# Kernel tuning notes

Hardware: AMD Instinct MI355X
Metric: run time of the kernel (lower is better)

Reference implementation:

```python
import jax, jax.numpy as jnp
import numpy as np

DEPTH = 6
IN_FEATURES = 256
NUM_TREES = 256
TREE_DIM = 1
BATCH = 2048


def sparsemax(X, axis=0):
    """Full-sort sparsemax projection along `axis` (k=None path of the torch code)."""
    X = jnp.moveaxis(X, axis, -1)
    Xs = X - jnp.max(X, axis=-1, keepdims=True)
    z = -jnp.sort(-Xs, axis=-1)                      # descending sort
    cs = jnp.cumsum(z, axis=-1) - 1.0                # topk_cumsum - 1
    d = X.shape[-1]
    rho = jnp.arange(1, d + 1, dtype=X.dtype)
    support = rho * z > cs
    k = jnp.sum(support, axis=-1, keepdims=True)     # support size (int)
    tau = jnp.take_along_axis(cs, k - 1, axis=-1) / k.astype(X.dtype)
    out = jnp.maximum(Xs - tau, 0.0)
    return jnp.moveaxis(out, -1, axis)


def sparsemoid(x):
    return jnp.clip(0.5 * x + 0.5, 0.0, 1.0)


def bin_codes_1hot(depth, dtype=jnp.float32):
    idx = jnp.arange(2 ** depth)
    off = 2 ** jnp.arange(depth)
    codes = ((idx[None, :] // off[:, None]) % 2).astype(dtype)   # [depth, 2^depth]
    return jnp.stack([codes, 1.0 - codes], axis=-1)              # [depth, 2^depth, 2]


def setup_inputs() -> dict:
    key = jax.random.key(0)
    k1, k2, k3, k4, k5 = jax.random.split(key, 5)
    x = jax.random.normal(k1, (BATCH, IN_FEATURES), dtype=jnp.float32)
    response = jax.random.normal(k2, (NUM_TREES, TREE_DIM, 2 ** DEPTH), dtype=jnp.float32)
    feature_selection_logits = jax.random.uniform(k3, (IN_FEATURES, NUM_TREES, DEPTH), dtype=jnp.float32)
    feature_thresholds = 0.5 * jax.random.normal(k4, (NUM_TREES, DEPTH), dtype=jnp.float32)
    log_temperatures = jnp.zeros((NUM_TREES, DEPTH), dtype=jnp.float32)
    return {
        "x": x,
        "response": response,
        "feature_selection_logits": feature_selection_logits,
        "feature_thresholds": feature_thresholds,
        "log_temperatures": log_temperatures,
    }


def reference(x, response, feature_selection_logits, feature_thresholds, log_temperatures):
    depth = feature_thresholds.shape[-1]
    codes = bin_codes_1hot(depth, x.dtype)                          # [d, 2^d, 2]
    # sparsemax feature routing over the feature axis
    fs = sparsemax(feature_selection_logits, axis=0)                # [F, T, d]
    fv = jnp.einsum('bi,ind->bnd', x, fs)                           # [B, T, d]
    tl = (fv - feature_thresholds) * jnp.exp(-log_temperatures)     # [B, T, d]
    bins = sparsemoid(jnp.stack([-tl, tl], axis=-1))                # [B, T, d, 2]
    bin_matches = jnp.einsum('btds,dcs->btdc', bins, codes)         # [B, T, d, 2^d]
    response_weights = jnp.prod(bin_matches, axis=-2)               # [B, T, 2^d]
    out = jnp.einsum('bnd,ncd->bnc', response_weights, response)    # [B, T, C]
    return out.reshape(out.shape[0], -1)                            # flatten_output=True
```

## Files before the change

### kernel.cpp

```cpp
#include <hip/hip_runtime.h>
#include <math.h>
#include <stdint.h>

#define NF 256
#define NT 256
#define ND 6
#define NB 2048
#define NCOL (NT * ND)
#define NLEAF 64

typedef __attribute__((ext_vector_type(8))) short bf16x8;
typedef __attribute__((ext_vector_type(4))) float f32x4;
typedef __attribute__((ext_vector_type(4))) unsigned short u16x4;

__device__ inline unsigned short f2bf(float f) {
    unsigned u = __float_as_uint(f);
    u += 0x7fffu + ((u >> 16) & 1u);
    return (unsigned short)(u >> 16);
}
__device__ inline float bf2f(unsigned short h) {
    return __uint_as_float(((unsigned)h) << 16);
}

__device__ inline void gld16(const void* g, void* l) {
    __builtin_amdgcn_global_load_lds(
        (const __attribute__((address_space(1))) unsigned int*)(uintptr_t)g,
        (__attribute__((address_space(3))) unsigned int*)(uintptr_t)l,
        16, 0, 0);
}

__global__ __launch_bounds__(256) void setup_kernel(
    const float* __restrict__ fsl,
    const float* __restrict__ x,
    const float* __restrict__ lt,
    unsigned short* __restrict__ fs_hi,
    unsigned short* __restrict__ fs_lo,
    unsigned short* __restrict__ x_hi,
    unsigned short* __restrict__ x_lo,
    float* __restrict__ scl)
{
    const int tid  = threadIdx.x;
    const int lane = tid & 63;
    const int col  = blockIdx.x * 4 + (tid >> 6);

    float xv[4];
    #pragma unroll
    for (int j = 0; j < 4; j++)
        xv[j] = fsl[(lane + 64 * j) * NCOL + col];

    float mx = fmaxf(fmaxf(xv[0], xv[1]), fmaxf(xv[2], xv[3]));
    #pragma unroll
    for (int off = 32; off > 0; off >>= 1)
        mx = fmaxf(mx, __shfl_xor(mx, off));
    #pragma unroll
    for (int j = 0; j < 4; j++) xv[j] -= mx;

    float s = (xv[0] + xv[1]) + (xv[2] + xv[3]);
    #pragma unroll
    for (int off = 32; off > 0; off >>= 1)
        s += __shfl_xor(s, off);
    float tau = (s - 1.0f) / 256.0f;

    int prev = 256;
    for (int it = 0; it < 64; it++) {
        float ss = 0.0f, cc = 0.0f;
        #pragma unroll
        for (int j = 0; j < 4; j++)
            if (xv[j] > tau) { ss += xv[j]; cc += 1.0f; }
        #pragma unroll
        for (int off = 32; off > 0; off >>= 1) {
            ss += __shfl_xor(ss, off);
            cc += __shfl_xor(cc, off);
        }
        const int c = (int)cc;
        if (c == prev) break;
        prev = c;
        tau = (ss - 1.0f) / cc;
    }

    #pragma unroll
    for (int j = 0; j < 4; j++) {
        const float v = fmaxf(xv[j] - tau, 0.0f);
        const unsigned short h = f2bf(v);
        fs_hi[col * NF + lane + 64 * j] = h;
        fs_lo[col * NF + lane + 64 * j] = f2bf(v - bf2f(h));
    }

    const int gid = blockIdx.x * 256 + tid;
    for (int e = gid; e < NB * NF / 4; e += (NCOL / 4) * 256) {
        const float4 v = ((const float4*)x)[e];
        const float vv[4] = {v.x, v.y, v.z, v.w};
        u16x4 h, l;
        #pragma unroll
        for (int j = 0; j < 4; j++) {
            h[j] = f2bf(vv[j]);
            l[j] = f2bf(vv[j] - bf2f(h[j]));
        }
        ((u16x4*)x_hi)[e] = h;
        ((u16x4*)x_lo)[e] = l;
    }

    if (gid < NT * ND) scl[gid] = __expf(-lt[gid]);
}

#define TM 64
#define TN 96
#define TK 32

struct MainBuf {
    unsigned short Ah[TM * TK];
    unsigned short Al[TM * TK];
    unsigned short Bh[TN * TK];
    unsigned short Bl[TN * TK];
};

union SMem {
    MainBuf mb[2];
    struct {
        float fv[TM][TN + 1];
        float resp[16][NLEAF + 4];
        float th[16 * ND];
        float sc[16 * ND];
    } ep;
};

__global__ __launch_bounds__(256) void gemm_tree_kernel(
    const unsigned short* __restrict__ x_hi,
    const unsigned short* __restrict__ x_lo,
    const unsigned short* __restrict__ fs_hi,
    const unsigned short* __restrict__ fs_lo,
    const float* __restrict__ thr,
    const float* __restrict__ scl,
    const float* __restrict__ resp_g,
    float* __restrict__ out)
{
    __shared__ SMem sm;

    const int tid  = threadIdx.x;
    const int lane = tid & 63;
    const int w    = tid >> 6;
    const int wm   = w & 1;
    const int wn   = w >> 1;
    const int bm0  = blockIdx.y * TM;
    const int bn0  = blockIdx.x * TN;
    const int t0   = blockIdx.x * 16;

    const int l15  = lane & 15;
    const int quad = lane >> 4;

    const int lr = lane >> 2;
    const int cp = lane & 3;

    const int rA  = (w << 4) + lr;
    const int cA  = cp ^ ((rA >> 1) & 3);
    const unsigned short* pAh = x_hi + (bm0 + rA) * NF + cA * 8;
    const unsigned short* pAl = x_lo + (bm0 + rA) * NF + cA * 8;

    const int s0  = w;
    const int rB0 = (s0 << 4) + lr;
    const int cB0 = cp ^ ((rB0 >> 1) & 3);
    const unsigned short* pBh0 = fs_hi + (bn0 + rB0) * NF + cB0 * 8;
    const unsigned short* pBl0 = fs_lo + (bn0 + rB0) * NF + cB0 * 8;
    const int s1  = w + 4;
    const int rB1 = (s1 << 4) + lr;
    const int cB1 = cp ^ ((rB1 >> 1) & 3);
    const unsigned short* pBh1 = fs_hi + (bn0 + rB1) * NF + cB1 * 8;
    const unsigned short* pBl1 = fs_lo + (bn0 + rB1) * NF + cB1 * 8;

    auto stage = [&](int kb, int k0) {
        MainBuf& b = sm.mb[kb];
        gld16(pAh + k0, &b.Ah[w << 9]);
        gld16(pAl + k0, &b.Al[w << 9]);
        gld16(pBh0 + k0, &b.Bh[s0 << 9]);
        gld16(pBl0 + k0, &b.Bl[s0 << 9]);
        if (w < 2) {
            gld16(pBh1 + k0, &b.Bh[s1 << 9]);
            gld16(pBl1 + k0, &b.Bl[s1 << 9]);
        }
    };

    f32x4 acc[2][3] = {};

    stage(0, 0);
    __syncthreads();

    #pragma unroll
    for (int t = 0; t < NF / TK; ++t) {
        const int kb = t & 1;
        if (t < NF / TK - 1) stage(kb ^ 1, (t + 1) * TK);

        MainBuf& b = sm.mb[kb];
        #pragma unroll
        for (int im = 0; im < 2; im++) {
            const int ar = wm * 32 + im * 16 + l15;
            const int sa = (quad ^ ((ar >> 1) & 3)) * 8;
            const bf16x8 a_h = *(const bf16x8*)&b.Ah[ar * TK + sa];
            const bf16x8 a_l = *(const bf16x8*)&b.Al[ar * TK + sa];
            #pragma unroll
            for (int in = 0; in < 3; in++) {
                const int br = wn * 48 + in * 16 + l15;
                const int sb = (quad ^ ((br >> 1) & 3)) * 8;
                const bf16x8 b_h = *(const bf16x8*)&b.Bh[br * TK + sb];
                const bf16x8 b_l = *(const bf16x8*)&b.Bl[br * TK + sb];
                acc[im][in] = __builtin_amdgcn_mfma_f32_16x16x32_bf16(a_h, b_h, acc[im][in], 0, 0, 0);
                acc[im][in] = __builtin_amdgcn_mfma_f32_16x16x32_bf16(a_h, b_l, acc[im][in], 0, 0, 0);
                acc[im][in] = __builtin_amdgcn_mfma_f32_16x16x32_bf16(a_l, b_h, acc[im][in], 0, 0, 0);
            }
        }
        __syncthreads();
    }

    #pragma unroll
    for (int im = 0; im < 2; im++)
        #pragma unroll
        for (int in = 0; in < 3; in++)
            #pragma unroll
            for (int r = 0; r < 4; r++) {
                const int m = wm * 32 + im * 16 + quad * 4 + r;
                const int n = wn * 48 + in * 16 + l15;
                sm.ep.fv[m][n] = acc[im][in][r];
            }
    {
        const int tr  = tid >> 4;
        const int seg = (tid & 15) * 4;
        *(f32x4*)&sm.ep.resp[tr][seg] = *(const f32x4*)&resp_g[(t0 + tr) * NLEAF + seg];
    }
    if (tid < 16 * ND)       sm.ep.th[tid]      = thr[t0 * ND + tid];
    else if (tid < 32 * ND)  sm.ep.sc[tid - 96] = scl[t0 * ND + tid - 96];
    __syncthreads();

    const int t16 = tid & 15;
    const int mr  = tid >> 4;
    #pragma unroll
    for (int i = 0; i < 4; i++) {
        const int m = mr + 16 * i;

        float sp[ND], sn[ND];
        #pragma unroll
        for (int d = 0; d < ND; d++) {
            const float f  = sm.ep.fv[m][t16 * ND + d];
            const float tl = (f - sm.ep.th[t16 * ND + d]) * sm.ep.sc[t16 * ND + d];
            const float h  = 0.5f * tl;
            sp[d] = fminf(fmaxf(0.5f + h, 0.0f), 1.0f);
            sn[d] = fminf(fmaxf(0.5f - h, 0.0f), 1.0f);
        }

        float r[32];
        #pragma unroll
        for (int c = 0; c < 32; c++)
            r[c] = sp[5] * sm.ep.resp[t16][c] + sn[5] * sm.ep.resp[t16][c + 32];
        #pragma unroll
        for (int d = 4; d >= 0; d--) {
            const int half = 1 << d;
            #pragma unroll
            for (int c = 0; c < 32; c++)
                if (c < half) r[c] = sp[d] * r[c] + sn[d] * r[c + half];
        }

        out[(bm0 + m) * NT + t0 + t16] = r[0];
    }
}

extern "C" void kernel_launch(void* const* d_in, const int* in_sizes, int n_in,
                              void* d_out, int out_size, void* d_ws, size_t ws_size,
                              hipStream_t stream)
{
    const float* x    = (const float*)d_in[0];
    const float* resp = (const float*)d_in[1];
    const float* fsl  = (const float*)d_in[2];
    const float* thr  = (const float*)d_in[3];
    const float* lt   = (const float*)d_in[4];
    float* out = (float*)d_out;

    unsigned short* fs_hi = (unsigned short*)d_ws;
    unsigned short* fs_lo = fs_hi + (size_t)NCOL * NF;
    unsigned short* x_hi  = fs_lo + (size_t)NCOL * NF;
    unsigned short* x_lo  = x_hi + (size_t)NB * NF;
    float*          scl   = (float*)(x_lo + (size_t)NB * NF);

    setup_kernel<<<NCOL / 4, 256, 0, stream>>>(fsl, x, lt, fs_hi, fs_lo, x_hi, x_lo, scl);

    dim3 g(NCOL / TN, NB / TM);
    gemm_tree_kernel<<<g, 256, 0, stream>>>(x_hi, x_lo, fs_hi, fs_lo, thr, scl, resp, out);
}
```

Measured before the change: 95.60 us.

## Stage GEMM tiles through registers with padded single-buffer LDS

```diff
diff --git a/kernel.cpp b/kernel.cpp
--- a/kernel.cpp
+++ b/kernel.cpp
@@ -11,6 +11,7 @@
 
 typedef __attribute__((ext_vector_type(8))) short bf16x8;
 typedef __attribute__((ext_vector_type(4))) float f32x4;
+typedef __attribute__((ext_vector_type(8))) unsigned short u16x8;
 typedef __attribute__((ext_vector_type(4))) unsigned short u16x4;
 
 __device__ inline unsigned short f2bf(float f) {
@@ -20,13 +21,6 @@
 }
 __device__ inline float bf2f(unsigned short h) {
     return __uint_as_float(((unsigned)h) << 16);
-}
-
-__device__ inline void gld16(const void* g, void* l) {
-    __builtin_amdgcn_global_load_lds(
-        (const __attribute__((address_space(1))) unsigned int*)(uintptr_t)g,
-        (__attribute__((address_space(3))) unsigned int*)(uintptr_t)l,
-        16, 0, 0);
 }
 
 __global__ __launch_bounds__(256) void setup_kernel(
@@ -106,16 +100,13 @@
 #define TM 64
 #define TN 96
 #define TK 32
-
-struct MainBuf {
-    unsigned short Ah[TM * TK];
-    unsigned short Al[TM * TK];
-    unsigned short Bh[TN * TK];
-    unsigned short Bl[TN * TK];
-};
+#define PK (TK + 8)
 
 union SMem {
-    MainBuf mb[2];
+    struct {
+        unsigned short Ah[TM][PK], Al[TM][PK];
+        unsigned short Bh[TN][PK], Bl[TN][PK];
+    } st;
     struct {
         float fv[TM][TN + 1];
         float resp[16][NLEAF + 4];
@@ -148,60 +139,49 @@
     const int l15  = lane & 15;
     const int quad = lane >> 4;
 
-    const int lr = lane >> 2;
-    const int cp = lane & 3;
-
-    const int rA  = (w << 4) + lr;
-    const int cA  = cp ^ ((rA >> 1) & 3);
-    const unsigned short* pAh = x_hi + (bm0 + rA) * NF + cA * 8;
-    const unsigned short* pAl = x_lo + (bm0 + rA) * NF + cA * 8;
-
-    const int s0  = w;
-    const int rB0 = (s0 << 4) + lr;
-    const int cB0 = cp ^ ((rB0 >> 1) & 3);
-    const unsigned short* pBh0 = fs_hi + (bn0 + rB0) * NF + cB0 * 8;
-    const unsigned short* pBl0 = fs_lo + (bn0 + rB0) * NF + cB0 * 8;
-    const int s1  = w + 4;
-    const int rB1 = (s1 << 4) + lr;
-    const int cB1 = cp ^ ((rB1 >> 1) & 3);
-    const unsigned short* pBh1 = fs_hi + (bn0 + rB1) * NF + cB1 * 8;
-    const unsigned short* pBl1 = fs_lo + (bn0 + rB1) * NF + cB1 * 8;
-
-    auto stage = [&](int kb, int k0) {
-        MainBuf& b = sm.mb[kb];
-        gld16(pAh + k0, &b.Ah[w << 9]);
-        gld16(pAl + k0, &b.Al[w << 9]);
-        gld16(pBh0 + k0, &b.Bh[s0 << 9]);
-        gld16(pBl0 + k0, &b.Bl[s0 << 9]);
-        if (w < 2) {
-            gld16(pBh1 + k0, &b.Bh[s1 << 9]);
-            gld16(pBl1 + k0, &b.Bl[s1 << 9]);
-        }
-    };
+    const int arow  = tid >> 2;
+    const int akseg = (tid & 3) * 8;
+    const int bhalf = tid >> 7;
+    const int brow  = (tid & 127) >> 2;
+    const int bkseg = (tid & 3) * 8;
+    const unsigned short* __restrict__ Bsrc = bhalf ? fs_lo : fs_hi;
+
+    u16x8 rAh, rAl, rB0, rB1, rB2;
+
+    #define LOAD_TILE(k0)                                                      \
+        do {                                                                   \
+            rAh = *(const u16x8*)&x_hi[(bm0 + arow) * NF + (k0) + akseg];      \
+            rAl = *(const u16x8*)&x_lo[(bm0 + arow) * NF + (k0) + akseg];      \
+            rB0 = *(const u16x8*)&Bsrc[(bn0 + brow) * NF + (k0) + bkseg];      \
+            rB1 = *(const u16x8*)&Bsrc[(bn0 + brow + 32) * NF + (k0) + bkseg]; \
+            rB2 = *(const u16x8*)&Bsrc[(bn0 + brow + 64) * NF + (k0) + bkseg]; \
+        } while (0)
 
     f32x4 acc[2][3] = {};
 
-    stage(0, 0);
-    __syncthreads();
-
-    #pragma unroll
+    LOAD_TILE(0);
+
     for (int t = 0; t < NF / TK; ++t) {
-        const int kb = t & 1;
-        if (t < NF / TK - 1) stage(kb ^ 1, (t + 1) * TK);
-
-        MainBuf& b = sm.mb[kb];
+        *(u16x8*)&sm.st.Ah[arow][akseg] = rAh;
+        *(u16x8*)&sm.st.Al[arow][akseg] = rAl;
+        {
+            unsigned short (*dst)[PK] = bhalf ? sm.st.Bl : sm.st.Bh;
+            *(u16x8*)&dst[brow][bkseg]      = rB0;
+            *(u16x8*)&dst[brow + 32][bkseg] = rB1;
+            *(u16x8*)&dst[brow + 64][bkseg] = rB2;
+        }
+        __syncthreads();
+
+        if (t < NF / TK - 1) LOAD_TILE((t + 1) * TK);
+
         #pragma unroll
         for (int im = 0; im < 2; im++) {
-            const int ar = wm * 32 + im * 16 + l15;
-            const int sa = (quad ^ ((ar >> 1) & 3)) * 8;
-            const bf16x8 a_h = *(const bf16x8*)&b.Ah[ar * TK + sa];
-            const bf16x8 a_l = *(const bf16x8*)&b.Al[ar * TK + sa];
+            const bf16x8 a_h = *(const bf16x8*)&sm.st.Ah[wm * 32 + im * 16 + l15][quad * 8];
+            const bf16x8 a_l = *(const bf16x8*)&sm.st.Al[wm * 32 + im * 16 + l15][quad * 8];
             #pragma unroll
             for (int in = 0; in < 3; in++) {
-                const int br = wn * 48 + in * 16 + l15;
-                const int sb = (quad ^ ((br >> 1) & 3)) * 8;
-                const bf16x8 b_h = *(const bf16x8*)&b.Bh[br * TK + sb];
-                const bf16x8 b_l = *(const bf16x8*)&b.Bl[br * TK + sb];
+                const bf16x8 b_h = *(const bf16x8*)&sm.st.Bh[wn * 48 + in * 16 + l15][quad * 8];
+                const bf16x8 b_l = *(const bf16x8*)&sm.st.Bl[wn * 48 + in * 16 + l15][quad * 8];
                 acc[im][in] = __builtin_amdgcn_mfma_f32_16x16x32_bf16(a_h, b_h, acc[im][in], 0, 0, 0);
                 acc[im][in] = __builtin_amdgcn_mfma_f32_16x16x32_bf16(a_h, b_l, acc[im][in], 0, 0, 0);
                 acc[im][in] = __builtin_amdgcn_mfma_f32_16x16x32_bf16(a_l, b_h, acc[im][in], 0, 0, 0);
```

After: 96.64 us. Within noise of the previous version (+1.1%).
